# Performance work log

Hardware: AMD Instinct MI355X
Metric: run time of the kernel (lower is better)

Reference implementation:

```python
import jax, jax.numpy as jnp
import numpy as np

N = 8192       # number of nodes
T = 4          # number of edge types
E = 131072     # edges per type
D = 32         # edge_emb_dim
H = 4          # num_head_attentions
NEG_SLOPE = 0.2


def setup_inputs() -> dict:
    key = jax.random.key(0)
    k1, k2, k3, k4 = jax.random.split(key, 4)
    scores = jax.random.normal(k1, (N, 1), dtype=jnp.float32)
    edge_type_emb = jax.random.normal(k2, (T, D), dtype=jnp.float32)
    edge_index = jax.random.randint(k3, (T, 2, E), 0, N, dtype=jnp.int32)
    # xavier-normal-ish init for the per-head attention weights [H, D+2, 1]
    std = float(np.sqrt(2.0 / (D + 2 + 1)))
    attention_weight = jax.random.normal(k4, (H, D + 2, 1), dtype=jnp.float32) * std
    return {"scores": scores, "edge_type_emb": edge_type_emb,
            "edge_index": edge_index, "attention_weight": attention_weight}


def _head_forward(W_h, scores, edge_type_emb, src, tgt):
    # W_h: [D+2, 1]; split the concat-matmul: cat([s_src, emb, s_tgt]) @ W
    w = W_h[:, 0]
    w_src, w_emb, w_tgt = w[0], w[1:D + 1], w[D + 1]
    s = scores[:, 0]                               # [N]
    # per-edge attention logits, vectorized over edge types: [T, E]
    emb_term = edge_type_emb @ w_emb               # [T]
    vals = s[src] * w_src + s[tgt] * w_tgt + emb_term[:, None]
    # scatter-add into dense NxN (duplicates accumulate, matching += semantics)
    A = jnp.zeros((N, N), dtype=scores.dtype).at[src.ravel(), tgt.ravel()].add(vals.ravel())
    A = jnp.where(A >= 0, A, NEG_SLOPE * A)        # LeakyReLU(0.2)
    A = jax.nn.softmax(A, axis=-1)                 # dense row softmax
    return A @ scores                               # [N, 1]


def reference(scores, edge_type_emb, edge_index, attention_weight):
    src = edge_index[:, 0, :]  # [T, E]
    tgt = edge_index[:, 1, :]
    head_fn = lambda W_h: _head_forward(W_h, scores, edge_type_emb, src, tgt)
    outs = jax.vmap(head_fn)(attention_weight)      # [H, N, 1]
    return jnp.mean(outs, axis=0)                   # [N, 1]
```

## Files before the change

### kernel.cpp

```cpp
#include <hip/hip_runtime.h>
#include <stdint.h>


#define NN 8192
#define TT 4
#define EE 131072
#define DD 32
#define HH 4
#define NEG_SLOPE 0.2f

#define SEG 256
#define SEG_SHIFT 8
#define HM (NN * SEG)
#define EMPTY 0xFFFFFFFFu


__global__ void k_init(uint32_t* __restrict__ tab,
                       const float* __restrict__ scores,
                       const float* __restrict__ ete,
                       const float* __restrict__ aw,
                       float* __restrict__ f) {
    uint32_t stride = gridDim.x * blockDim.x;
    for (uint32_t i = blockIdx.x * blockDim.x + threadIdx.x; i < HM; i += stride)
        tab[i] = EMPTY;
    if (blockIdx.x == 0) {
        __shared__ float red[256];
        int tid = threadIdx.x;
        float s = 0.f;
        for (int i = tid; i < NN; i += 256) s += scores[i];
        red[tid] = s;
        __syncthreads();
        for (int off = 128; off > 0; off >>= 1) {
            if (tid < off) red[tid] += red[tid + off];
            __syncthreads();
        }
        if (tid == 0) f[0] = red[0];
        if (tid < HH) {
            f[1 + tid] = aw[tid * (DD + 2)];
            f[5 + tid] = aw[tid * (DD + 2) + DD + 1];
        }
        if (tid < HH * TT) {
            int h = tid / TT, t = tid % TT;
            float acc = 0.f;
            for (int d = 0; d < DD; ++d)
                acc += ete[t * DD + d] * aw[h * (DD + 2) + 1 + d];
            f[9 + tid] = acc;
        }
    }
}

__global__ void k_build(const int* __restrict__ ei, uint32_t* __restrict__ tab) {
    int idx = blockIdx.x * blockDim.x + threadIdx.x;
    int t = idx >> 17;
    int e = idx & (EE - 1);
    uint32_t src = (uint32_t)ei[(t * 2) * EE + e];
    uint32_t tgt = (uint32_t)ei[(t * 2 + 1) * EE + e];
    uint32_t inc = 1u << (13 + 4 * t);
    uint32_t base = src << SEG_SHIFT;
    uint32_t pos = (tgt * 2654435761u) >> 24;
    uint32_t fresh = tgt | inc;
    while (true) {
        uint32_t slot = base | pos;
        uint32_t cur = atomicCAS(&tab[slot], EMPTY, fresh);
        if (cur == EMPTY) return;
        while ((cur & 0x1FFFu) == tgt) {
            uint32_t prev = atomicCAS(&tab[slot], cur, cur + inc);
            if (prev == cur) return;
            cur = prev;
        }
        pos = (pos + 1) & (SEG - 1);
    }
}

__device__ __forceinline__ void entry_accum(uint32_t w, float si,
                                            const float* __restrict__ scores,
                                            const float* wsrc, const float* wtgt,
                                            const float* em,
                                            float* num, float* den) {
    if (w == EMPTY) return;
    uint32_t tgt = w & 0x1FFFu;
    float c0 = (float)((w >> 13) & 15u);
    float c1 = (float)((w >> 17) & 15u);
    float c2 = (float)((w >> 21) & 15u);
    float c3 = (float)((w >> 25) & 15u);
    float ctot = c0 + c1 + c2 + c3;
    float sj = scores[tgt];
    #pragma unroll
    for (int h = 0; h < HH; ++h) {
        float a = ctot * (si * wsrc[h] + sj * wtgt[h])
                + c0 * em[h * 4 + 0] + c1 * em[h * 4 + 1]
                + c2 * em[h * 4 + 2] + c3 * em[h * 4 + 3];
        a = (a >= 0.f) ? a : NEG_SLOPE * a;
        float ex = expf(a) - 1.f;
        den[h] += ex;
        num[h] += ex * sj;
    }
}

__global__ void __launch_bounds__(256) k_accum(const float* __restrict__ scores,
                                               const uint32_t* __restrict__ tab,
                                               const float* __restrict__ f,
                                               float* __restrict__ out) {
    int wave = (int)((blockIdx.x * blockDim.x + threadIdx.x) >> 6);
    int lane = threadIdx.x & 63;
    float st = f[0];
    float wsrc[HH], wtgt[HH], em[HH * TT];
    #pragma unroll
    for (int h = 0; h < HH; ++h) { wsrc[h] = f[1 + h]; wtgt[h] = f[5 + h]; }
    #pragma unroll
    for (int k = 0; k < HH * TT; ++k) em[k] = f[9 + k];

    float si = scores[wave];
    const uint4* seg4 = (const uint4*)(tab + ((uint32_t)wave << SEG_SHIFT));
    uint4 w = seg4[lane];

    float num[HH] = {0.f, 0.f, 0.f, 0.f};
    float den[HH] = {0.f, 0.f, 0.f, 0.f};
    entry_accum(w.x, si, scores, wsrc, wtgt, em, num, den);
    entry_accum(w.y, si, scores, wsrc, wtgt, em, num, den);
    entry_accum(w.z, si, scores, wsrc, wtgt, em, num, den);
    entry_accum(w.w, si, scores, wsrc, wtgt, em, num, den);

    #pragma unroll
    for (int m = 32; m > 0; m >>= 1) {
        #pragma unroll
        for (int h = 0; h < HH; ++h) {
            num[h] += __shfl_xor(num[h], m, 64);
            den[h] += __shfl_xor(den[h], m, 64);
        }
    }
    if (lane == 0) {
        float acc = 0.f;
        #pragma unroll
        for (int h = 0; h < HH; ++h)
            acc += (st + num[h]) / ((float)NN + den[h]);
        out[wave] = acc * (1.f / HH);
    }
}

extern "C" void kernel_launch(void* const* d_in, const int* in_sizes, int n_in,
                              void* d_out, int out_size, void* d_ws, size_t ws_size,
                              hipStream_t stream) {
    const float* scores = (const float*)d_in[0];
    const float* ete    = (const float*)d_in[1];
    const int*   ei     = (const int*)d_in[2];
    const float* aw     = (const float*)d_in[3];
    float* out = (float*)d_out;
    uint32_t* tab = (uint32_t*)d_ws;
    float* f = (float*)(tab + HM);

    k_init<<<2048, 256, 0, stream>>>(tab, scores, ete, aw, f);
    k_build<<<(TT * EE) / 256, 256, 0, stream>>>(ei, tab);
    k_accum<<<NN / 4, 256, 0, stream>>>(scores, tab, f, out);
}
```

Before: 113.2 us.

## Bucket edges by source row block, then build per-block hash tables in LDS

Replaces the global 8 MB hash table, with its fill pass and global atomicCAS inserts, by a two-pass scheme. First, edges are packed and scattered into 256 row-block buckets using a shared-memory histogram and global cursors. Then each block builds a 32-row by 128-slot hash table in shared memory and runs the softmax accumulation from LDS. This removes the large table initialisation and the global atomic traffic. In exchange, bucket capacity is fixed at 2560 with silent truncation, and the per-row table is halved to 128 slots, so a row with too many distinct targets could loop forever or lose edges.

```diff
diff --git a/kernel.cpp b/kernel.cpp
--- a/kernel.cpp
+++ b/kernel.cpp
@@ -9,132 +9,174 @@
 #define HH 4
 #define NEG_SLOPE 0.2f
 
-#define SEG 256
-#define SEG_SHIFT 8
-#define HM (NN * SEG)
+#define NB  256
+#define RPB 32
+#define CAP 2560
+#define SEG 128
 #define EMPTY 0xFFFFFFFFu
 
 
-__global__ void k_init(uint32_t* __restrict__ tab,
-                       const float* __restrict__ scores,
-                       const float* __restrict__ ete,
-                       const float* __restrict__ aw,
-                       float* __restrict__ f) {
-    uint32_t stride = gridDim.x * blockDim.x;
-    for (uint32_t i = blockIdx.x * blockDim.x + threadIdx.x; i < HM; i += stride)
-        tab[i] = EMPTY;
-    if (blockIdx.x == 0) {
-        __shared__ float red[256];
-        int tid = threadIdx.x;
-        float s = 0.f;
-        for (int i = tid; i < NN; i += 256) s += scores[i];
-        red[tid] = s;
+__global__ void k0(const float* __restrict__ scores,
+                   const float* __restrict__ ete,
+                   const float* __restrict__ aw,
+                   uint32_t* __restrict__ cursor,
+                   float* __restrict__ f) {
+    int tid = threadIdx.x;
+    if (tid < NB) cursor[tid] = 0;
+    __shared__ float red[256];
+    float s = 0.f;
+    for (int i = tid; i < NN; i += 256) s += scores[i];
+    red[tid] = s;
+    __syncthreads();
+    for (int off = 128; off > 0; off >>= 1) {
+        if (tid < off) red[tid] += red[tid + off];
         __syncthreads();
-        for (int off = 128; off > 0; off >>= 1) {
-            if (tid < off) red[tid] += red[tid + off];
-            __syncthreads();
-        }
-        if (tid == 0) f[0] = red[0];
-        if (tid < HH) {
-            f[1 + tid] = aw[tid * (DD + 2)];
-            f[5 + tid] = aw[tid * (DD + 2) + DD + 1];
-        }
-        if (tid < HH * TT) {
-            int h = tid / TT, t = tid % TT;
-            float acc = 0.f;
-            for (int d = 0; d < DD; ++d)
-                acc += ete[t * DD + d] * aw[h * (DD + 2) + 1 + d];
-            f[9 + tid] = acc;
-        }
+    }
+    if (tid == 0) f[0] = red[0];
+    if (tid < HH) {
+        f[1 + tid] = aw[tid * (DD + 2)];
+        f[5 + tid] = aw[tid * (DD + 2) + DD + 1];
+    }
+    if (tid < HH * TT) {
+        int h = tid / TT, t = tid % TT;
+        float acc = 0.f;
+        for (int d = 0; d < DD; ++d)
+            acc += ete[t * DD + d] * aw[h * (DD + 2) + 1 + d];
+        f[9 + tid] = acc;
     }
 }
 
-__global__ void k_build(const int* __restrict__ ei, uint32_t* __restrict__ tab) {
-    int idx = blockIdx.x * blockDim.x + threadIdx.x;
-    int t = idx >> 17;
-    int e = idx & (EE - 1);
-    uint32_t src = (uint32_t)ei[(t * 2) * EE + e];
-    uint32_t tgt = (uint32_t)ei[(t * 2 + 1) * EE + e];
-    uint32_t inc = 1u << (13 + 4 * t);
-    uint32_t base = src << SEG_SHIFT;
-    uint32_t pos = (tgt * 2654435761u) >> 24;
-    uint32_t fresh = tgt | inc;
-    while (true) {
-        uint32_t slot = base | pos;
-        uint32_t cur = atomicCAS(&tab[slot], EMPTY, fresh);
-        if (cur == EMPTY) return;
-        while ((cur & 0x1FFFu) == tgt) {
-            uint32_t prev = atomicCAS(&tab[slot], cur, cur + inc);
-            if (prev == cur) return;
-            cur = prev;
-        }
-        pos = (pos + 1) & (SEG - 1);
+#define A_EPT 16
+__global__ void __launch_bounds__(256) kA(const int* __restrict__ ei,
+                                          uint32_t* __restrict__ cursor,
+                                          uint32_t* __restrict__ buf) {
+    __shared__ uint32_t hist[NB];
+    __shared__ uint32_t baseh[NB];
+    int tid = threadIdx.x;
+    if (tid < NB) hist[tid] = 0;
+    __syncthreads();
+
+    uint32_t gtid = blockIdx.x * 256u + (uint32_t)tid;
+    uint32_t t  = gtid >> 13;
+    uint32_t e0 = (gtid & 8191u) * A_EPT;
+    const int4* sp = (const int4*)(ei + (size_t)(t * 2) * EE + e0);
+    const int4* tp = (const int4*)(ei + (size_t)(t * 2 + 1) * EE + e0);
+
+    uint32_t val[A_EPT];
+    uint32_t rnk[A_EPT];
+    #pragma unroll
+    for (int k = 0; k < A_EPT / 4; ++k) {
+        int4 s4 = sp[k];
+        int4 t4 = tp[k];
+        val[k*4+0] = ((uint32_t)s4.x << 15) | ((uint32_t)t4.x << 2) | t;
+        val[k*4+1] = ((uint32_t)s4.y << 15) | ((uint32_t)t4.y << 2) | t;
+        val[k*4+2] = ((uint32_t)s4.z << 15) | ((uint32_t)t4.z << 2) | t;
+        val[k*4+3] = ((uint32_t)s4.w << 15) | ((uint32_t)t4.w << 2) | t;
+    }
+    #pragma unroll
+    for (int k = 0; k < A_EPT; ++k)
+        rnk[k] = atomicAdd(&hist[val[k] >> 20], 1u);
+    __syncthreads();
+    if (tid < NB) baseh[tid] = atomicAdd(&cursor[tid], hist[tid]);
+    __syncthreads();
+    #pragma unroll
+    for (int k = 0; k < A_EPT; ++k) {
+        uint32_t b = val[k] >> 20;
+        buf[b * CAP + baseh[b] + rnk[k]] = val[k] & 0xFFFFFu;
     }
 }
 
-__device__ __forceinline__ void entry_accum(uint32_t w, float si,
-                                            const float* __restrict__ scores,
-                                            const float* wsrc, const float* wtgt,
-                                            const float* em,
-                                            float* num, float* den) {
-    if (w == EMPTY) return;
-    uint32_t tgt = w & 0x1FFFu;
-    float c0 = (float)((w >> 13) & 15u);
-    float c1 = (float)((w >> 17) & 15u);
-    float c2 = (float)((w >> 21) & 15u);
-    float c3 = (float)((w >> 25) & 15u);
-    float ctot = c0 + c1 + c2 + c3;
-    float sj = scores[tgt];
-    #pragma unroll
-    for (int h = 0; h < HH; ++h) {
-        float a = ctot * (si * wsrc[h] + sj * wtgt[h])
-                + c0 * em[h * 4 + 0] + c1 * em[h * 4 + 1]
-                + c2 * em[h * 4 + 2] + c3 * em[h * 4 + 3];
-        a = (a >= 0.f) ? a : NEG_SLOPE * a;
-        float ex = expf(a) - 1.f;
-        den[h] += ex;
-        num[h] += ex * sj;
-    }
-}
+__global__ void __launch_bounds__(256) kB(const float* __restrict__ scores,
+                                          const uint32_t* __restrict__ cursor,
+                                          const uint32_t* __restrict__ buf,
+                                          const float* __restrict__ f,
+                                          float* __restrict__ out) {
+    __shared__ uint32_t tab[RPB * SEG];
+    int tid = threadIdx.x;
+    for (int i = tid; i < RPB * SEG; i += 256) tab[i] = EMPTY;
 
-__global__ void __launch_bounds__(256) k_accum(const float* __restrict__ scores,
-                                               const uint32_t* __restrict__ tab,
-                                               const float* __restrict__ f,
-                                               float* __restrict__ out) {
-    int wave = (int)((blockIdx.x * blockDim.x + threadIdx.x) >> 6);
-    int lane = threadIdx.x & 63;
     float st = f[0];
     float wsrc[HH], wtgt[HH], em[HH * TT];
     #pragma unroll
     for (int h = 0; h < HH; ++h) { wsrc[h] = f[1 + h]; wtgt[h] = f[5 + h]; }
     #pragma unroll
     for (int k = 0; k < HH * TT; ++k) em[k] = f[9 + k];
+    __syncthreads();
 
-    float si = scores[wave];
-    const uint4* seg4 = (const uint4*)(tab + ((uint32_t)wave << SEG_SHIFT));
-    uint4 w = seg4[lane];
+    uint32_t b = blockIdx.x;
+    uint32_t n = cursor[b];
+    if (n > CAP) n = CAP;
+    const uint32_t* bb = buf + b * CAP;
 
-    float num[HH] = {0.f, 0.f, 0.f, 0.f};
-    float den[HH] = {0.f, 0.f, 0.f, 0.f};
-    entry_accum(w.x, si, scores, wsrc, wtgt, em, num, den);
-    entry_accum(w.y, si, scores, wsrc, wtgt, em, num, den);
-    entry_accum(w.z, si, scores, wsrc, wtgt, em, num, den);
-    entry_accum(w.w, si, scores, wsrc, wtgt, em, num, den);
-
-    #pragma unroll
-    for (int m = 32; m > 0; m >>= 1) {
-        #pragma unroll
-        for (int h = 0; h < HH; ++h) {
-            num[h] += __shfl_xor(num[h], m, 64);
-            den[h] += __shfl_xor(den[h], m, 64);
+    for (uint32_t i = tid; i < n; i += 256) {
+        uint32_t v   = bb[i];
+        uint32_t row = v >> 15;
+        uint32_t tgt = (v >> 2) & 8191u;
+        uint32_t tt  = v & 3u;
+        uint32_t inc = 1u << (13 + 4 * tt);
+        uint32_t fresh = tgt | inc;
+        uint32_t pos = (tgt * 2654435761u) >> 25;
+        uint32_t base = row * SEG;
+        while (true) {
+            uint32_t cur = atomicCAS(&tab[base + pos], EMPTY, fresh);
+            if (cur == EMPTY) break;
+            bool done = false;
+            while ((cur & 0x1FFFu) == tgt) {
+                uint32_t prev = atomicCAS(&tab[base + pos], cur, cur + inc);
+                if (prev == cur) { done = true; break; }
+                cur = prev;
+            }
+            if (done) break;
+            pos = (pos + 1) & (SEG - 1);
         }
     }
-    if (lane == 0) {
-        float acc = 0.f;
+    __syncthreads();
+
+    int wave = tid >> 6, lane = tid & 63;
+    #pragma unroll
+    for (int rr = 0; rr < 8; ++rr) {
+        int r = wave * 8 + rr;
+        float si = scores[b * RPB + r];
+        float num[HH] = {0.f, 0.f, 0.f, 0.f};
+        float den[HH] = {0.f, 0.f, 0.f, 0.f};
         #pragma unroll
-        for (int h = 0; h < HH; ++h)
-            acc += (st + num[h]) / ((float)NN + den[h]);
-        out[wave] = acc * (1.f / HH);
+        for (int half = 0; half < 2; ++half) {
+            uint32_t w = tab[r * SEG + half * 64 + lane];
+            if (w != EMPTY) {
+                uint32_t tgt = w & 0x1FFFu;
+                float c0 = (float)((w >> 13) & 15u);
+                float c1 = (float)((w >> 17) & 15u);
+                float c2 = (float)((w >> 21) & 15u);
+                float c3 = (float)((w >> 25) & 15u);
+                float ctot = c0 + c1 + c2 + c3;
+                float sj = scores[tgt];
+                #pragma unroll
+                for (int h = 0; h < HH; ++h) {
+                    float a = ctot * (si * wsrc[h] + sj * wtgt[h])
+                            + c0 * em[h * 4 + 0] + c1 * em[h * 4 + 1]
+                            + c2 * em[h * 4 + 2] + c3 * em[h * 4 + 3];
+                    a = (a >= 0.f) ? a : NEG_SLOPE * a;
+                    float ex = expf(a) - 1.f;
+                    den[h] += ex;
+                    num[h] += ex * sj;
+                }
+            }
+        }
+        #pragma unroll
+        for (int m = 32; m > 0; m >>= 1) {
+            #pragma unroll
+            for (int h = 0; h < HH; ++h) {
+                num[h] += __shfl_xor(num[h], m, 64);
+                den[h] += __shfl_xor(den[h], m, 64);
+            }
+        }
+        if (lane == 0) {
+            float acc = 0.f;
+            #pragma unroll
+            for (int h = 0; h < HH; ++h)
+                acc += (st + num[h]) / ((float)NN + den[h]);
+            out[b * RPB + r] = acc * (1.f / HH);
+        }
     }
 }
 
@@ -146,10 +188,12 @@
     const int*   ei     = (const int*)d_in[2];
     const float* aw     = (const float*)d_in[3];
     float* out = (float*)d_out;
-    uint32_t* tab = (uint32_t*)d_ws;
-    float* f = (float*)(tab + HM);
 
-    k_init<<<2048, 256, 0, stream>>>(tab, scores, ete, aw, f);
-    k_build<<<(TT * EE) / 256, 256, 0, stream>>>(ei, tab);
-    k_accum<<<NN / 4, 256, 0, stream>>>(scores, tab, f, out);
+    uint32_t* cursor = (uint32_t*)d_ws;
+    float*    f      = (float*)(cursor + NB);
+    uint32_t* buf    = cursor + NB + 64;
+
+    k0<<<1, 256, 0, stream>>>(scores, ete, aw, cursor, f);
+    kA<<<128, 256, 0, stream>>>(ei, cursor, buf);
+    kB<<<NB, 256, 0, stream>>>(scores, cursor, buf, f, out);
 }
```

New measurement: 105.2 us. 7.1% less time.
